# Kernel tuning notes

Measured on AMD Instinct MI355X. Metric: run time of the kernel, lower is better.

## Reference

```python
import jax, jax.numpy as jnp
import numpy as np

# Instant-NGP HashGrid constants (match tcnn encoding_config defaults in the module)
N_LEVELS = 16
N_FEATS = 2
LOG2_T = 16
T = 1 << LOG2_T            # hashmap entries per level
BASE_RES = 16
PER_LEVEL_SCALE = 1.5
N_POINTS = 1 << 20
PRIMES = (1, 2654435761, 805459861)  # tcnn spatial-hash primes

# 8 corner offsets of the unit cube, [8,3]
_CORNERS = np.array([[i, j, k] for i in (0, 1) for j in (0, 1) for k in (0, 1)], dtype=np.float32)


def setup_inputs() -> dict:
    key = jax.random.key(0)
    k1, k2 = jax.random.split(key)
    x = jax.random.uniform(k1, (N_POINTS, 3), dtype=jnp.float32)
    # tcnn initializes hash tables uniform in [-1e-4, 1e-4]
    table = jax.random.uniform(k2, (N_LEVELS, T, N_FEATS), minval=-1e-4, maxval=1e-4, dtype=jnp.float32)
    return {"x": x, "table": table}


def _corner_index(grid, res, dense):
    # grid: [N,8,3] int32 corner coordinates -> [N,8] table index
    if dense:
        g = jnp.clip(grid, 0, res - 1)
        return g[..., 0] + g[..., 1] * res + g[..., 2] * res * res
    g = grid.astype(jnp.uint32)
    h = (g[..., 0] * jnp.uint32(PRIMES[0])
         ^ g[..., 1] * jnp.uint32(PRIMES[1])
         ^ g[..., 2] * jnp.uint32(PRIMES[2]))
    return (h & jnp.uint32(T - 1)).astype(jnp.int32)


def _hashgrid_forward(x, table):
    x = x.astype(jnp.float32)
    offs = jnp.asarray(_CORNERS)                      # [8,3]
    outs = []
    for level in range(N_LEVELS):
        # tcnn: grid_scale = base * s^level - 1 ; resolution = ceil(scale)+1
        scale = float(BASE_RES * (PER_LEVEL_SCALE ** level) - 1.0)
        res = int(np.ceil(scale)) + 1
        dense = res ** 3 <= T                          # tcnn uses dense indexing when the grid fits
        pos = x * scale + 0.5                          # [N,3]
        g0 = jnp.floor(pos)
        frac = pos - g0                                # [N,3] trilinear fractions
        grid = (g0[:, None, :] + offs[None]).astype(jnp.int32)   # [N,8,3]
        idx = _corner_index(grid, res, dense)          # [N,8]
        feat = table[level][idx]                       # [N,8,F] irregular gather
        # trilinear weights: prod over dims of frac or (1-frac) per corner
        w = jnp.prod(jnp.where(offs[None] > 0, frac[:, None, :], 1.0 - frac[:, None, :]), axis=-1)  # [N,8]
        outs.append(jnp.sum(w[..., None] * feat, axis=1))        # [N,F]
    return jnp.concatenate(outs, axis=-1)              # [N, L*F] = [N,32]


def reference(x, table):
    return _hashgrid_forward(x, table)
```

## Files before the change

### kernel.cpp

```cpp
#include <hip/hip_runtime.h>
#include <stdint.h>


#define NLVL 16
#define TS 65536
#define P2 2654435761u
#define P3 805459861u

typedef float v4f __attribute__((ext_vector_type(4)));
typedef float v2f __attribute__((ext_vector_type(2)));
typedef float v4fa8 __attribute__((ext_vector_type(4), aligned(8)));

__constant__ float C_SCALES[NLVL] = {
    15.0f, 23.0f, 35.0f, 53.0f, 80.0f, 120.5f, 181.25f, 272.375f,
    409.0625f, 614.09375f, 921.640625f, 1382.9609375f,
    2074.94140625f, 3112.912109375f, 4669.8681640625f, 7005.30224609375f};

__device__ __forceinline__ v2f v4lo(v4f v) { v2f r; r.x = v.x; r.y = v.y; return r; }
__device__ __forceinline__ v2f v4hi(v4f v) { v2f r; r.x = v.z; r.y = v.w; return r; }
__device__ __forceinline__ v2f v4lo8(v4fa8 v) { v2f r; r.x = v.x; r.y = v.y; return r; }
__device__ __forceinline__ v2f v4hi8(v4fa8 v) { v2f r; r.x = v.z; r.y = v.w; return r; }

__device__ __forceinline__ void lds_put2(float* s, int p, int gl, int h,
                                         float a, float b) {
    const int slot = (gl + p) & 3;
    const int a32 = p * 16 + slot * 4 + h * 2;
    s[a32] = a;
    s[a32 + 1] = b;
}

__device__ __forceinline__ v2f hashed_level(float px, float py, float pz,
                                            float scale, const v2f* tbl) {
    const float fx = px * scale + 0.5f;
    const float fy = py * scale + 0.5f;
    const float fz = pz * scale + 0.5f;
    const float gx = floorf(fx), gy = floorf(fy), gz = floorf(fz);
    const float wx = fx - gx, wy = fy - gy, wz = fz - gz;
    const int ix = (int)gx, iy = (int)gy, iz = (int)gz;

    const uint32_t bx = (uint32_t)ix;
    const uint32_t hy0 = (uint32_t)iy * P2, hy1 = hy0 + P2;
    const uint32_t hz0 = (uint32_t)iz * P3, hz1 = hz0 + P3;
    const uint32_t b00 = hy0 ^ hz0, b01 = hy0 ^ hz1;
    const uint32_t b10 = hy1 ^ hz0, b11 = hy1 ^ hz1;
    const uint32_t i00 = (bx ^ b00) & (TS - 1);
    const uint32_t i01 = (bx ^ b01) & (TS - 1);
    const uint32_t i10 = (bx ^ b10) & (TS - 1);
    const uint32_t i11 = (bx ^ b11) & (TS - 1);
    const v4f* tbl4 = (const v4f*)tbl;
    const v4f f00 = tbl4[i00 >> 1];
    const v4f f01 = tbl4[i01 >> 1];
    const v4f f10 = tbl4[i10 >> 1];
    const v4f f11 = tbl4[i11 >> 1];
    const v2f c0 = (i00 & 1) ? v4hi(f00) : v4lo(f00);
    const v2f c1 = (i01 & 1) ? v4hi(f01) : v4lo(f01);
    const v2f c2 = (i10 & 1) ? v4hi(f10) : v4lo(f10);
    const v2f c3 = (i11 & 1) ? v4hi(f11) : v4lo(f11);
    v2f c4, c5, c6, c7;
    if ((ix & 1) == 0) {
        c4 = (i00 & 1) ? v4lo(f00) : v4hi(f00);
        c5 = (i01 & 1) ? v4lo(f01) : v4hi(f01);
        c6 = (i10 & 1) ? v4lo(f10) : v4hi(f10);
        c7 = (i11 & 1) ? v4lo(f11) : v4hi(f11);
    } else {
        const uint32_t bx1 = bx + 1;
        c4 = tbl[(bx1 ^ b00) & (TS - 1)];
        c5 = tbl[(bx1 ^ b01) & (TS - 1)];
        c6 = tbl[(bx1 ^ b10) & (TS - 1)];
        c7 = tbl[(bx1 ^ b11) & (TS - 1)];
    }

    const float ux = 1.0f - wx, uy = 1.0f - wy, uz = 1.0f - wz;
    const float w0 = ux * uy * uz, w1 = ux * uy * wz;
    const float w2 = ux * wy * uz, w3 = ux * wy * wz;
    const float w4 = wx * uy * uz, w5 = wx * uy * wz;
    const float w6 = wx * wy * uz, w7 = wx * wy * wz;

    v2f o;
    o.x = w0 * c0.x + w1 * c1.x + w2 * c2.x + w3 * c3.x +
          w4 * c4.x + w5 * c5.x + w6 * c6.x + w7 * c7.x;
    o.y = w0 * c0.y + w1 * c1.y + w2 * c2.y + w3 * c3.y +
          w4 * c4.y + w5 * c5.y + w6 * c6.y + w7 * c7.y;
    return o;
}

__global__ __launch_bounds__(256, 8) void hashgrid_fwd(
    const float* __restrict__ x,
    const float* __restrict__ table,
    float* __restrict__ out,
    int n)
{
    __shared__ float s_out[256 * 16];

    const int tid0 = blockIdx.x * 256 + threadIdx.x;
    const int tid = min(tid0, n - 1);
    const int p = threadIdx.x;

    const float px = x[3 * tid + 0];
    const float py = x[3 * tid + 1];
    const float pz = x[3 * tid + 2];

    v4f* outb4 = (v4f*)out + (size_t)blockIdx.x * (256 * 8);
    const long long lim4 = (long long)n * 8 - (long long)blockIdx.x * (256 * 8);

    {
        const int RESO[3] = {16, 24, 36};
        const float DSC[3] = {15.0f, 23.0f, 35.0f};
#pragma unroll
        for (int l = 0; l < 3; ++l) {
            const float scale = DSC[l];
            const float fx = px * scale + 0.5f;
            const float fy = py * scale + 0.5f;
            const float fz = pz * scale + 0.5f;
            const float gx = floorf(fx), gy = floorf(fy), gz = floorf(fz);
            const float wx = fx - gx, wy = fy - gy, wz = fz - gz;
            const int ix = (int)gx, iy = (int)gy, iz = (int)gz;

            const v2f* tbl = ((const v2f*)table) + (size_t)l * TS;
            const int R = RESO[l];
            const int x0 = min(ix, R - 1);
            const int y0 = min(iy, R - 1), y1 = min(iy + 1, R - 1);
            const int z0 = min(iz, R - 1), z1 = min(iz + 1, R - 1);
            const int xb = min(x0, R - 2);
            const bool hi0 = (x0 != xb);
            const int y0R = y0 * R, y1R = y1 * R;
            const int z0R = z0 * R * R, z1R = z1 * R * R;
            const v4fa8 f00 = *(const v4fa8*)(tbl + (xb + y0R + z0R));
            const v4fa8 f01 = *(const v4fa8*)(tbl + (xb + y0R + z1R));
            const v4fa8 f10 = *(const v4fa8*)(tbl + (xb + y1R + z0R));
            const v4fa8 f11 = *(const v4fa8*)(tbl + (xb + y1R + z1R));
            const v2f c0 = hi0 ? v4hi8(f00) : v4lo8(f00), c4 = v4hi8(f00);
            const v2f c1 = hi0 ? v4hi8(f01) : v4lo8(f01), c5 = v4hi8(f01);
            const v2f c2 = hi0 ? v4hi8(f10) : v4lo8(f10), c6 = v4hi8(f10);
            const v2f c3 = hi0 ? v4hi8(f11) : v4lo8(f11), c7 = v4hi8(f11);

            const float ux = 1.0f - wx, uy = 1.0f - wy, uz = 1.0f - wz;
            const float w0 = ux * uy * uz, w1 = ux * uy * wz;
            const float w2 = ux * wy * uz, w3 = ux * wy * wz;
            const float w4 = wx * uy * uz, w5 = wx * uy * wz;
            const float w6 = wx * wy * uz, w7 = wx * wy * wz;

            const float o0 = w0 * c0.x + w1 * c1.x + w2 * c2.x + w3 * c3.x +
                             w4 * c4.x + w5 * c5.x + w6 * c6.x + w7 * c7.x;
            const float o1 = w0 * c0.y + w1 * c1.y + w2 * c2.y + w3 * c3.y +
                             w4 * c4.y + w5 * c5.y + w6 * c6.y + w7 * c7.y;
            lds_put2(s_out, p, l >> 1, l & 1, o0, o1);
        }
    }
#pragma unroll 2
    for (int l = 3; l < 8; ++l) {
        const v2f o = hashed_level(px, py, pz, C_SCALES[l],
                                   ((const v2f*)table) + (size_t)l * TS);
        lds_put2(s_out, p, l >> 1, l & 1, o.x, o.y);
    }
    __syncthreads();
#pragma unroll
    for (int r = 0; r < 4; ++r) {
        const int e = r * 256 + threadIdx.x;
        const int pp = e >> 2, g = e & 3;
        const int slot = (g + pp) & 3;
        const v4f v = *(const v4f*)&s_out[pp * 16 + slot * 4];
        const int o4 = pp * 8 + g;
        if (o4 < lim4) outb4[o4] = v;
    }
    __syncthreads();

#pragma unroll 2
    for (int l = 8; l < NLVL; ++l) {
        const v2f o = hashed_level(px, py, pz, C_SCALES[l],
                                   ((const v2f*)table) + (size_t)l * TS);
        lds_put2(s_out, p, (l >> 1) - 4, l & 1, o.x, o.y);
    }
    __syncthreads();
#pragma unroll
    for (int r = 0; r < 4; ++r) {
        const int e = r * 256 + threadIdx.x;
        const int pp = e >> 2, g = e & 3;
        const int slot = (g + pp) & 3;
        const v4f v = *(const v4f*)&s_out[pp * 16 + slot * 4];
        const int o4 = pp * 8 + 4 + g;
        if (o4 < lim4) outb4[o4] = v;
    }
}

extern "C" void kernel_launch(void* const* d_in, const int* in_sizes, int n_in,
                              void* d_out, int out_size, void* d_ws, size_t ws_size,
                              hipStream_t stream) {
    const float* x = (const float*)d_in[0];
    const float* table = (const float*)d_in[1];
    float* out = (float*)d_out;
    const int n = in_sizes[0] / 3;
    const int block = 256;
    const int grid = (n + block - 1) / block;
    hashgrid_fwd<<<grid, block, 0, stream>>>(x, table, out, n);
}
```

Before: 500.9 us.

## Split hashgrid forward into two kernels for low and high levels

Splits the single kernel into two launches: one computes levels 0-7 and writes the first half of each output row, the other computes levels 8-15 and writes the second half. Each kernel touches only half of the hash tables, so the working set of table data per launch is smaller and more of it may stay in cache. In exchange the point coordinates are read twice, and there is an extra launch plus a serialisation point between the two kernels.

```diff
diff --git a/kernel.cpp b/kernel.cpp
--- a/kernel.cpp
+++ b/kernel.cpp
@@ -84,7 +84,7 @@
     return o;
 }
 
-__global__ __launch_bounds__(256, 8) void hashgrid_fwd(
+__global__ __launch_bounds__(256, 8) void hashgrid_fwd_lo(
     const float* __restrict__ x,
     const float* __restrict__ table,
     float* __restrict__ out,
@@ -100,8 +100,10 @@
     const float py = x[3 * tid + 1];
     const float pz = x[3 * tid + 2];
 
-    v4f* outb4 = (v4f*)out + (size_t)blockIdx.x * (256 * 8);
-    const long long lim4 = (long long)n * 8 - (long long)blockIdx.x * (256 * 8);
+    v4f* outb4 = (v4f*)out + (size_t)blockIdx.x * 2048;
+    const long long lim4 = (long long)n * 8 - (long long)blockIdx.x * 2048;
+
+    const v2f* tblv = (const v2f*)table;
 
     {
         const int RESO[3] = {16, 24, 36};
@@ -116,7 +118,7 @@
             const float wx = fx - gx, wy = fy - gy, wz = fz - gz;
             const int ix = (int)gx, iy = (int)gy, iz = (int)gz;
 
-            const v2f* tbl = ((const v2f*)table) + (size_t)l * TS;
+            const v2f* tbl = tblv + (size_t)l * TS;
             const int R = RESO[l];
             const int x0 = min(ix, R - 1);
             const int y0 = min(iy, R - 1), y1 = min(iy + 1, R - 1);
@@ -150,7 +152,7 @@
 #pragma unroll 2
     for (int l = 3; l < 8; ++l) {
         const v2f o = hashed_level(px, py, pz, C_SCALES[l],
-                                   ((const v2f*)table) + (size_t)l * TS);
+                                   tblv + (size_t)l * TS);
         lds_put2(s_out, p, l >> 1, l & 1, o.x, o.y);
     }
     __syncthreads();
@@ -163,12 +165,33 @@
         const int o4 = pp * 8 + g;
         if (o4 < lim4) outb4[o4] = v;
     }
-    __syncthreads();
+}
+
+__global__ __launch_bounds__(256, 8) void hashgrid_fwd_hi(
+    const float* __restrict__ x,
+    const float* __restrict__ table,
+    float* __restrict__ out,
+    int n)
+{
+    __shared__ float s_out[256 * 16];
+
+    const int tid0 = blockIdx.x * 256 + threadIdx.x;
+    const int tid = min(tid0, n - 1);
+    const int p = threadIdx.x;
+
+    const float px = x[3 * tid + 0];
+    const float py = x[3 * tid + 1];
+    const float pz = x[3 * tid + 2];
+
+    v4f* outb4 = (v4f*)out + (size_t)blockIdx.x * 2048;
+    const long long lim4 = (long long)n * 8 - (long long)blockIdx.x * 2048;
+
+    const v2f* tblv = (const v2f*)table;
 
 #pragma unroll 2
     for (int l = 8; l < NLVL; ++l) {
         const v2f o = hashed_level(px, py, pz, C_SCALES[l],
-                                   ((const v2f*)table) + (size_t)l * TS);
+                                   tblv + (size_t)l * TS);
         lds_put2(s_out, p, (l >> 1) - 4, l & 1, o.x, o.y);
     }
     __syncthreads();
@@ -192,5 +215,6 @@
     const int n = in_sizes[0] / 3;
     const int block = 256;
     const int grid = (n + block - 1) / block;
-    hashgrid_fwd<<<grid, block, 0, stream>>>(x, table, out, n);
-}
+    hashgrid_fwd_lo<<<grid, block, 0, stream>>>(x, table, out, n);
+    hashgrid_fwd_hi<<<grid, block, 0, stream>>>(x, table, out, n);
+}
```

Measured after the change: 488.2 us. -2.5%, faster.
